# Kernel tuning notes

Hardware: AMD Instinct MI355X
Metric: run time of the kernel (lower is better)

Reference implementation:

```python
import jax, jax.numpy as jnp
import numpy as np

NEI_SIZE = [16]  # matches init kwarg nei_size

def setup_inputs() -> dict:
    key = jax.random.key(0)
    k = jax.random.split(key, 5)
    B, N, S = 512, 32, 16
    EF, NF = 64, 128
    return {
        "x": jax.random.normal(k[0], (B, N, NF), dtype=jnp.float32),
        "x_nei_rel": jax.random.normal(k[1], (B, N * S, EF), dtype=jnp.float32),
        "x_nei_node": jax.random.normal(k[2], (B, N * S, NF), dtype=jnp.float32),
        "W1_w": jax.random.normal(k[3], (NF, EF + NF), dtype=jnp.float32) * 0.05,
        "W1_b": jax.random.normal(k[4], (NF,), dtype=jnp.float32) * 0.05,
        "i": 0,
    }

def reference(x, x_nei_rel, x_nei_node, W1_w, W1_b, i):
    S = NEI_SIZE[i]                       # now_nei_size (static python int)
    B, N, D = x.shape                     # N = n_neibor, D = nodeFea
    norm = 1.0 / np.sqrt(D).astype(np.float32)
    # concat edge+node feats and project: [B, N*S, EF+NF] -> [B, N*S, D]
    x_nei = jnp.concatenate([x_nei_rel, x_nei_node], axis=-1)
    v = (x_nei @ W1_w.T + W1_b).reshape(B, N, S, D)
    # per-node attention over its S neighbors
    alpha = jnp.einsum('bnd,bnsd->bns', x, v) * norm   # [B, N, S]
    alpha = jax.nn.softmax(alpha, axis=-1)
    # weighted neighbor sum
    return jnp.einsum('bns,bnsd->bnd', alpha, v)       # [B, N, D]
```

## Files before the change

kernel.cpp:

```cpp
#include <hip/hip_runtime.h>
#include <stdint.h>


typedef __attribute__((ext_vector_type(8))) short short8;
typedef __attribute__((ext_vector_type(4))) float float4_t;
typedef __attribute__((ext_vector_type(4))) unsigned short ushort4_t;

#define GRID_ 1024
#define ITERS_ 16

__device__ __forceinline__ unsigned short f2bf(float f) {
    uint32_t u = __float_as_uint(f);
    u += 0x7fffu + ((u >> 16) & 1u);
    return (unsigned short)(u >> 16);
}

__device__ __forceinline__ int aoff(int s, int kc) {
    return (((kc >> 5) * 64) + (((kc & 31) >> 3) * 16) + s) * 8 + (kc & 7);
}

__global__ __launch_bounds__(256) void nei_attn_kernel(
    const float* __restrict__ x,
    const float* __restrict__ rel,
    const float* __restrict__ node,
    const float* __restrict__ W,
    const float* __restrict__ bias,
    float* __restrict__ out)
{
    __shared__ __align__(16) unsigned short lds_a[6 * 64 * 8];
    __shared__ float lds_x[128];
    __shared__ float lds_v[16 * 132];
    __shared__ float lds_ap[256];
    __shared__ float lds_alpha[16];

    const int t    = threadIdx.x;
    const int lane = t & 63;
    const int wv   = t >> 6;
    const int l15  = lane & 15;
    const int quad = lane >> 4;

    short8 bf0[6], bf1[6];
    const int row0 = wv * 32 + l15;
    const int row1 = row0 + 16;
    const float bias0 = bias[row0];
    const float bias1 = bias[row1];
    #pragma unroll
    for (int q = 0; q < 6; ++q) {
        const float* p0 = W + row0 * 192 + q * 32 + quad * 8;
        const float* p1 = W + row1 * 192 + q * 32 + quad * 8;
        float4_t a0 = *(const float4_t*)p0;
        float4_t a1 = *(const float4_t*)(p0 + 4);
        float4_t c0 = *(const float4_t*)p1;
        float4_t c1 = *(const float4_t*)(p1 + 4);
        short8 f0, f1;
        f0[0] = (short)f2bf(a0.x); f0[1] = (short)f2bf(a0.y);
        f0[2] = (short)f2bf(a0.z); f0[3] = (short)f2bf(a0.w);
        f0[4] = (short)f2bf(a1.x); f0[5] = (short)f2bf(a1.y);
        f0[6] = (short)f2bf(a1.z); f0[7] = (short)f2bf(a1.w);
        f1[0] = (short)f2bf(c0.x); f1[1] = (short)f2bf(c0.y);
        f1[2] = (short)f2bf(c0.z); f1[3] = (short)f2bf(c0.w);
        f1[4] = (short)f2bf(c1.x); f1[5] = (short)f2bf(c1.y);
        f1[6] = (short)f2bf(c1.z); f1[7] = (short)f2bf(c1.w);
        bf0[q] = f0; bf1[q] = f1;
    }

    const int s0 = t >> 4,       kc0 = (t & 15) << 2;
    const int s1 = t >> 5,       kc1 = 64 + ((t & 31) << 2);
    const int s2 = s1 + 8;
    const int ao0 = aoff(s0, kc0);
    const int ao1 = aoff(s1, kc1);
    const int ao2 = aoff(s2, kc1);

    int idx = blockIdx.x * ITERS_;

    float4_t pf0, pf1, pf2, pfx;
    {
        const float* pr = rel  + idx * 1024;
        const float* pn = node + idx * 2048;
        pf0 = *(const float4_t*)(pr + t * 4);
        pf1 = *(const float4_t*)(pn + t * 4);
        pf2 = *(const float4_t*)(pn + 1024 + t * 4);
        if (t < 32) pfx = *(const float4_t*)(x + idx * 128 + t * 4);
    }

    for (int it = 0; it < ITERS_; ++it) {
        {
            ushort4_t u;
            u[0] = f2bf(pf0.x); u[1] = f2bf(pf0.y); u[2] = f2bf(pf0.z); u[3] = f2bf(pf0.w);
            *(ushort4_t*)&lds_a[ao0] = u;
            u[0] = f2bf(pf1.x); u[1] = f2bf(pf1.y); u[2] = f2bf(pf1.z); u[3] = f2bf(pf1.w);
            *(ushort4_t*)&lds_a[ao1] = u;
            u[0] = f2bf(pf2.x); u[1] = f2bf(pf2.y); u[2] = f2bf(pf2.z); u[3] = f2bf(pf2.w);
            *(ushort4_t*)&lds_a[ao2] = u;
            if (t < 32) *(float4_t*)&lds_x[t * 4] = pfx;
        }
        __syncthreads();

        if (it + 1 < ITERS_) {
            const int nidx = idx + 1;
            const float* pr = rel  + nidx * 1024;
            const float* pn = node + nidx * 2048;
            pf0 = *(const float4_t*)(pr + t * 4);
            pf1 = *(const float4_t*)(pn + t * 4);
            pf2 = *(const float4_t*)(pn + 1024 + t * 4);
            if (t < 32) pfx = *(const float4_t*)(x + nidx * 128 + t * 4);
        }

        float4_t acc0 = {0.f, 0.f, 0.f, 0.f};
        float4_t acc1 = {0.f, 0.f, 0.f, 0.f};
        #pragma unroll
        for (int q = 0; q < 6; ++q) {
            short8 af = *(const short8*)&lds_a[(q * 64 + lane) * 8];
            acc0 = __builtin_amdgcn_mfma_f32_16x16x32_bf16(af, bf0[q], acc0, 0, 0, 0);
            acc1 = __builtin_amdgcn_mfma_f32_16x16x32_bf16(af, bf1[q], acc1, 0, 0, 0);
        }

        const int col0 = wv * 32 + l15;
        const int rb = quad * 4;
        #pragma unroll
        for (int r = 0; r < 4; ++r) {
            lds_v[(rb + r) * 132 + col0]      = acc0[r] + bias0;
            lds_v[(rb + r) * 132 + col0 + 16] = acc1[r] + bias1;
        }
        __syncthreads();

        {
            const int sA = t >> 4, dA = t & 15;
            float p = 0.f;
            #pragma unroll
            for (int j = 0; j < 8; ++j) {
                const int d = dA + (j << 4);
                p += lds_x[d] * lds_v[sA * 132 + d];
            }
            lds_ap[t] = p;
        }
        __syncthreads();

        if (t < 16) {
            float a = 0.f;
            #pragma unroll
            for (int j = 0; j < 16; ++j) a += lds_ap[t * 16 + j];
            lds_alpha[t] = a * 0.08838834764831845f;
        }
        __syncthreads();

        if (t < 128) {
            float m = lds_alpha[0];
            #pragma unroll
            for (int s = 1; s < 16; ++s) m = fmaxf(m, lds_alpha[s]);
            float e[16], den = 0.f;
            #pragma unroll
            for (int s = 0; s < 16; ++s) { e[s] = __expf(lds_alpha[s] - m); den += e[s]; }
            float o = 0.f;
            #pragma unroll
            for (int s = 0; s < 16; ++s) o += e[s] * lds_v[s * 132 + t];
            out[idx * 128 + t] = o / den;
        }
        ++idx;
    }
}

extern "C" void kernel_launch(void* const* d_in, const int* in_sizes, int n_in,
                              void* d_out, int out_size, void* d_ws, size_t ws_size,
                              hipStream_t stream) {
    const float* x    = (const float*)d_in[0];
    const float* rel  = (const float*)d_in[1];
    const float* node = (const float*)d_in[2];
    const float* W    = (const float*)d_in[3];
    const float* bias = (const float*)d_in[4];
    float* out = (float*)d_out;
    hipLaunchKernelGGL(nei_attn_kernel, dim3(GRID_), dim3(256), 0, stream,
                       x, rel, node, W, bias, out);
}
```

Measured before the change: 265.1 us.

## Process two nodes per iteration with 512-thread blocks and shuffle reductions

Each block now runs 512 threads. The two halves of the block stage two nodes' neighbour tiles into double-sized LDS buffers, and each of the 8 waves computes 16 output columns for both nodes with a shared W fragment. This halves the per-wave W registers and doubles the loads in flight per block. The alpha dot-product reduction now uses wavefront xor-shuffles instead of an LDS partial array and a separate reduction stage, which removes one barrier per iteration. The cost is larger LDS use and 512-thread barriers, and the occupancy hint may limit registers.

```diff
diff --git a/kernel.cpp b/kernel.cpp
--- a/kernel.cpp
+++ b/kernel.cpp
@@ -7,7 +7,7 @@
 typedef __attribute__((ext_vector_type(4))) unsigned short ushort4_t;
 
 #define GRID_ 1024
-#define ITERS_ 16
+#define ITERS_ 8
 
 __device__ __forceinline__ unsigned short f2bf(float f) {
     uint32_t u = __float_as_uint(f);
@@ -19,7 +19,7 @@
     return (((kc >> 5) * 64) + (((kc & 31) >> 3) * 16) + s) * 8 + (kc & 7);
 }
 
-__global__ __launch_bounds__(256) void nei_attn_kernel(
+__global__ __launch_bounds__(512, 8) void nei_attn_kernel(
     const float* __restrict__ x,
     const float* __restrict__ rel,
     const float* __restrict__ node,
@@ -27,136 +27,128 @@
     const float* __restrict__ bias,
     float* __restrict__ out)
 {
-    __shared__ __align__(16) unsigned short lds_a[6 * 64 * 8];
-    __shared__ float lds_x[128];
-    __shared__ float lds_v[16 * 132];
-    __shared__ float lds_ap[256];
-    __shared__ float lds_alpha[16];
+    __shared__ __align__(16) unsigned short lds_a[2][6 * 64 * 8];
+    __shared__ float lds_x[2][128];
+    __shared__ float lds_v[2][16 * 132];
+    __shared__ float lds_alpha[2][16];
 
     const int t    = threadIdx.x;
+    const int tl   = t & 255;
+    const int h    = t >> 8;
     const int lane = t & 63;
     const int wv   = t >> 6;
     const int l15  = lane & 15;
-    const int quad = lane >> 4;
+    const int quad = (lane >> 4) & 3;
 
-    short8 bf0[6], bf1[6];
-    const int row0 = wv * 32 + l15;
-    const int row1 = row0 + 16;
-    const float bias0 = bias[row0];
-    const float bias1 = bias[row1];
+    short8 bf[6];
+    const int row = wv * 16 + l15;
+    const float bias_c = bias[row];
     #pragma unroll
     for (int q = 0; q < 6; ++q) {
-        const float* p0 = W + row0 * 192 + q * 32 + quad * 8;
-        const float* p1 = W + row1 * 192 + q * 32 + quad * 8;
-        float4_t a0 = *(const float4_t*)p0;
-        float4_t a1 = *(const float4_t*)(p0 + 4);
-        float4_t c0 = *(const float4_t*)p1;
-        float4_t c1 = *(const float4_t*)(p1 + 4);
-        short8 f0, f1;
-        f0[0] = (short)f2bf(a0.x); f0[1] = (short)f2bf(a0.y);
-        f0[2] = (short)f2bf(a0.z); f0[3] = (short)f2bf(a0.w);
-        f0[4] = (short)f2bf(a1.x); f0[5] = (short)f2bf(a1.y);
-        f0[6] = (short)f2bf(a1.z); f0[7] = (short)f2bf(a1.w);
-        f1[0] = (short)f2bf(c0.x); f1[1] = (short)f2bf(c0.y);
-        f1[2] = (short)f2bf(c0.z); f1[3] = (short)f2bf(c0.w);
-        f1[4] = (short)f2bf(c1.x); f1[5] = (short)f2bf(c1.y);
-        f1[6] = (short)f2bf(c1.z); f1[7] = (short)f2bf(c1.w);
-        bf0[q] = f0; bf1[q] = f1;
+        const float* p = W + row * 192 + q * 32 + quad * 8;
+        float4_t a0 = *(const float4_t*)p;
+        float4_t a1 = *(const float4_t*)(p + 4);
+        short8 f;
+        f[0] = (short)f2bf(a0.x); f[1] = (short)f2bf(a0.y);
+        f[2] = (short)f2bf(a0.z); f[3] = (short)f2bf(a0.w);
+        f[4] = (short)f2bf(a1.x); f[5] = (short)f2bf(a1.y);
+        f[6] = (short)f2bf(a1.z); f[7] = (short)f2bf(a1.w);
+        bf[q] = f;
     }
 
-    const int s0 = t >> 4,       kc0 = (t & 15) << 2;
-    const int s1 = t >> 5,       kc1 = 64 + ((t & 31) << 2);
+    const int s0 = tl >> 4,  kc0 = (tl & 15) << 2;
+    const int s1 = tl >> 5,  kc1 = 64 + ((tl & 31) << 2);
     const int s2 = s1 + 8;
-    const int ao0 = aoff(s0, kc0);
-    const int ao1 = aoff(s1, kc1);
-    const int ao2 = aoff(s2, kc1);
+    const int ao0 = h * 3072 + aoff(s0, kc0);
+    const int ao1 = h * 3072 + aoff(s1, kc1);
+    const int ao2 = h * 3072 + aoff(s2, kc1);
+    unsigned short* la = &lds_a[0][0];
 
-    int idx = blockIdx.x * ITERS_;
+    int idx = blockIdx.x * (ITERS_ * 2);
 
-    float4_t pf0, pf1, pf2, pfx;
+    float4_t pf0, pf1, pf2;
+    float pfx = 0.f;
     {
-        const float* pr = rel  + idx * 1024;
-        const float* pn = node + idx * 2048;
-        pf0 = *(const float4_t*)(pr + t * 4);
-        pf1 = *(const float4_t*)(pn + t * 4);
-        pf2 = *(const float4_t*)(pn + 1024 + t * 4);
-        if (t < 32) pfx = *(const float4_t*)(x + idx * 128 + t * 4);
+        const float* pr = rel  + (idx + h) * 1024;
+        const float* pn = node + (idx + h) * 2048;
+        pf0 = *(const float4_t*)(pr + tl * 4);
+        pf1 = *(const float4_t*)(pn + tl * 4);
+        pf2 = *(const float4_t*)(pn + 1024 + tl * 4);
+        if (t < 256) pfx = x[(idx + (t >> 7)) * 128 + (t & 127)];
     }
 
     for (int it = 0; it < ITERS_; ++it) {
         {
             ushort4_t u;
             u[0] = f2bf(pf0.x); u[1] = f2bf(pf0.y); u[2] = f2bf(pf0.z); u[3] = f2bf(pf0.w);
-            *(ushort4_t*)&lds_a[ao0] = u;
+            *(ushort4_t*)&la[ao0] = u;
             u[0] = f2bf(pf1.x); u[1] = f2bf(pf1.y); u[2] = f2bf(pf1.z); u[3] = f2bf(pf1.w);
-            *(ushort4_t*)&lds_a[ao1] = u;
+            *(ushort4_t*)&la[ao1] = u;
             u[0] = f2bf(pf2.x); u[1] = f2bf(pf2.y); u[2] = f2bf(pf2.z); u[3] = f2bf(pf2.w);
-            *(ushort4_t*)&lds_a[ao2] = u;
-            if (t < 32) *(float4_t*)&lds_x[t * 4] = pfx;
+            *(ushort4_t*)&la[ao2] = u;
+            if (t < 256) lds_x[t >> 7][t & 127] = pfx;
         }
         __syncthreads();
 
         if (it + 1 < ITERS_) {
-            const int nidx = idx + 1;
-            const float* pr = rel  + nidx * 1024;
-            const float* pn = node + nidx * 2048;
-            pf0 = *(const float4_t*)(pr + t * 4);
-            pf1 = *(const float4_t*)(pn + t * 4);
-            pf2 = *(const float4_t*)(pn + 1024 + t * 4);
-            if (t < 32) pfx = *(const float4_t*)(x + nidx * 128 + t * 4);
+            const int nidx = idx + 2;
+            const float* pr = rel  + (nidx + h) * 1024;
+            const float* pn = node + (nidx + h) * 2048;
+            pf0 = *(const float4_t*)(pr + tl * 4);
+            pf1 = *(const float4_t*)(pn + tl * 4);
+            pf2 = *(const float4_t*)(pn + 1024 + tl * 4);
+            if (t < 256) pfx = x[(nidx + (t >> 7)) * 128 + (t & 127)];
         }
 
         float4_t acc0 = {0.f, 0.f, 0.f, 0.f};
         float4_t acc1 = {0.f, 0.f, 0.f, 0.f};
         #pragma unroll
         for (int q = 0; q < 6; ++q) {
-            short8 af = *(const short8*)&lds_a[(q * 64 + lane) * 8];
-            acc0 = __builtin_amdgcn_mfma_f32_16x16x32_bf16(af, bf0[q], acc0, 0, 0, 0);
-            acc1 = __builtin_amdgcn_mfma_f32_16x16x32_bf16(af, bf1[q], acc1, 0, 0, 0);
+            short8 af0 = *(const short8*)&la[(q * 64 + lane) * 8];
+            short8 af1 = *(const short8*)&la[3072 + (q * 64 + lane) * 8];
+            acc0 = __builtin_amdgcn_mfma_f32_16x16x32_bf16(af0, bf[q], acc0, 0, 0, 0);
+            acc1 = __builtin_amdgcn_mfma_f32_16x16x32_bf16(af1, bf[q], acc1, 0, 0, 0);
         }
-
-        const int col0 = wv * 32 + l15;
+        const int colw = wv * 16 + l15;
         const int rb = quad * 4;
         #pragma unroll
         for (int r = 0; r < 4; ++r) {
-            lds_v[(rb + r) * 132 + col0]      = acc0[r] + bias0;
-            lds_v[(rb + r) * 132 + col0 + 16] = acc1[r] + bias1;
+            lds_v[0][(rb + r) * 132 + colw] = acc0[r] + bias_c;
+            lds_v[1][(rb + r) * 132 + colw] = acc1[r] + bias_c;
         }
         __syncthreads();
 
         {
-            const int sA = t >> 4, dA = t & 15;
+            const int sA = tl >> 4, dA = tl & 15;
             float p = 0.f;
             #pragma unroll
             for (int j = 0; j < 8; ++j) {
                 const int d = dA + (j << 4);
-                p += lds_x[d] * lds_v[sA * 132 + d];
+                p += lds_x[h][d] * lds_v[h][sA * 132 + d];
             }
-            lds_ap[t] = p;
+            p += __shfl_xor(p, 8);
+            p += __shfl_xor(p, 4);
+            p += __shfl_xor(p, 2);
+            p += __shfl_xor(p, 1);
+            if (dA == 0) lds_alpha[h][sA] = p * 0.08838834764831845f;
         }
         __syncthreads();
 
-        if (t < 16) {
-            float a = 0.f;
+        if (tl < 128) {
+            const float* al = lds_alpha[h];
+            float m = al[0];
             #pragma unroll
-            for (int j = 0; j < 16; ++j) a += lds_ap[t * 16 + j];
-            lds_alpha[t] = a * 0.08838834764831845f;
+            for (int s = 1; s < 16; ++s) m = fmaxf(m, al[s]);
+            float den = 0.f, o = 0.f;
+            #pragma unroll
+            for (int s = 0; s < 16; ++s) {
+                const float e = __expf(al[s] - m);
+                den += e;
+                o += e * lds_v[h][s * 132 + tl];
+            }
+            out[(idx + h) * 128 + tl] = o / den;
         }
-        __syncthreads();
-
-        if (t < 128) {
-            float m = lds_alpha[0];
-            #pragma unroll
-            for (int s = 1; s < 16; ++s) m = fmaxf(m, lds_alpha[s]);
-            float e[16], den = 0.f;
-            #pragma unroll
-            for (int s = 0; s < 16; ++s) { e[s] = __expf(lds_alpha[s] - m); den += e[s]; }
-            float o = 0.f;
-            #pragma unroll
-            for (int s = 0; s < 16; ++s) o += e[s] * lds_v[s * 132 + t];
-            out[idx * 128 + t] = o / den;
-        }
-        ++idx;
+        idx += 2;
     }
 }
 
@@ -169,6 +161,6 @@
     const float* W    = (const float*)d_in[3];
     const float* bias = (const float*)d_in[4];
     float* out = (float*)d_out;
-    hipLaunchKernelGGL(nei_attn_kernel, dim3(GRID_), dim3(256), 0, stream,
+    hipLaunchKernelGGL(nei_attn_kernel, dim3(GRID_), dim3(512), 0, stream,
                        x, rel, node, W, bias, out);
 }
```

After: 305.6 us. 15.3% more time.
